# Performance work log

Hardware: AMD Instinct MI355X
Metric: run time of the kernel (lower is better)

The kernel has to match this reference:

```python
import jax, jax.numpy as jnp
import numpy as np
from jax import lax

EPS = 1e-8  # torch F.cosine_similarity default eps


def setup_inputs() -> dict:
    key = jax.random.key(0)
    k1, k2, k3 = jax.random.split(key, 3)
    B, S, D_in, D_out, W = 256, 10, 4096, 4096, 5
    x = jax.random.normal(k1, (B, S, D_in), dtype=jnp.float32)
    # Conv1d weight [out_channels, in_channels, kernel] with PyTorch-style init scale
    fan_in = D_in * W
    conv_w = jax.random.normal(k2, (D_out, D_in, W), dtype=jnp.float32) / np.sqrt(fan_in)
    conv_b = jax.random.normal(k3, (D_out,), dtype=jnp.float32) / np.sqrt(fan_in)
    return {"x": x, "conv_w": conv_w, "conv_b": conv_b}


def _cosine_weight(x):
    # x: [B, S, D]; central frame index = S//2 + 1 (as in the original code)
    S = x.shape[1]
    c = S // 2 + 1
    central = x[:, c, :]                               # [B, D]
    dots = jnp.einsum("bsd,bd->bs", x, central)        # [B, S]
    norms = jnp.sqrt(jnp.sum(x * x, axis=-1))          # [B, S]
    cnorm = norms[:, c]                                # [B]
    denom = jnp.maximum(norms, EPS) * jnp.maximum(cnorm, EPS)[:, None]
    w = dots / denom                                   # [B, S] (raw weights; normalization in source is dead code)
    return x * w[..., None]                            # [B, S, D]


def reference(x, conv_w, conv_b):
    xw = _cosine_weight(x)                             # [B, S, D_in]
    xc = jnp.transpose(xw, (0, 2, 1))                  # [B, D_in, S]
    y = lax.conv_general_dilated(
        xc, conv_w, window_strides=(1,), padding="VALID",
        dimension_numbers=("NCH", "OIH", "NCH"),
    )                                                  # [B, D_out, S-W+1]
    y = y + conv_b[None, :, None]
    return jnp.mean(y, axis=-1)                        # [B, D_out]
```

## Files before the change

### kernel.cpp

```cpp
#include <hip/hip_runtime.h>
#include <hip/hip_bf16.h>

typedef __hip_bfloat16 bf16;
typedef __attribute__((ext_vector_type(8))) __bf16 bf16x8;
typedef __attribute__((ext_vector_type(4))) __bf16 bf16x4;
typedef __attribute__((ext_vector_type(4))) float f32x4;

typedef const __attribute__((address_space(1))) void cgvoid;
typedef __attribute__((address_space(3))) void lvoid;

constexpr int B_ = 256, S_ = 10, D_ = 4096, W_ = 5;
constexpr int K_ = D_ * W_;
constexpr int M_ = 256, N_ = 4096;
constexpr int KS_ = 8;
constexpr int KPER = K_ / KS_;
constexpr int BK_ = 32;
constexpr int ITERS = KPER / BK_;
constexpr int TN_ = 64;
constexpr float EPSV = 1e-8f;

__global__ void detect_kernel(const unsigned short* __restrict__ xr, int* __restrict__ flag){
    int lane = threadIdx.x;
    int sane = 0;
    for (int i = lane; i < 2048; i += 64){
        unsigned short u = xr[i];
        int e = (u >> 7) & 0xFF;
        if ((e >= 97 && e <= 137) || ((u & 0x7FFF) == 0)) sane++;
    }
    #pragma unroll
    for (int off = 32; off > 0; off >>= 1) sane += __shfl_down(sane, off);
    if (lane == 0) *flag = (sane >= 1536) ? 1 : 0;
}

__global__ __launch_bounds__(512) void zw_kernel(const void* __restrict__ xv,
                                                 bf16* __restrict__ Z,
                                                 const int* __restrict__ flag){
    const bool isb = (*flag != 0);
    int b = blockIdx.x, t = threadIdx.x;
    int i0 = t * 8;
    float f[S_][8];
    if (isb){
        const __bf16* xb = (const __bf16*)xv + (size_t)b * S_ * D_ + i0;
        #pragma unroll
        for (int s = 0; s < S_; ++s){
            bf16x8 v = *(const bf16x8*)(xb + s * D_);
            #pragma unroll
            for (int j = 0; j < 8; ++j) f[s][j] = (float)v[j];
        }
    } else {
        const float* xb = (const float*)xv + (size_t)b * S_ * D_ + i0;
        #pragma unroll
        for (int s = 0; s < S_; ++s){
            float4 a = *(const float4*)(xb + s * D_);
            float4 c = *(const float4*)(xb + s * D_ + 4);
            f[s][0]=a.x; f[s][1]=a.y; f[s][2]=a.z; f[s][3]=a.w;
            f[s][4]=c.x; f[s][5]=c.y; f[s][6]=c.z; f[s][7]=c.w;
        }
    }
    float dsum[S_], nsum[S_];
    #pragma unroll
    for (int s = 0; s < S_; ++s){
        float d = 0.f, n = 0.f;
        #pragma unroll
        for (int j = 0; j < 8; ++j){ d += f[s][j] * f[6][j]; n += f[s][j] * f[s][j]; }
        dsum[s] = d; nsum[s] = n;
    }
    int lane = t & 63, wv = t >> 6;
    #pragma unroll
    for (int s = 0; s < S_; ++s){
        #pragma unroll
        for (int off = 32; off > 0; off >>= 1){
            dsum[s] += __shfl_down(dsum[s], off);
            nsum[s] += __shfl_down(nsum[s], off);
        }
    }
    __shared__ float sd[8][S_], sn[8][S_], wsh[S_];
    if (lane == 0){
        #pragma unroll
        for (int s = 0; s < S_; ++s){ sd[wv][s] = dsum[s]; sn[wv][s] = nsum[s]; }
    }
    __syncthreads();
    if (t < S_){
        float Dv = 0.f, Nv = 0.f;
        #pragma unroll
        for (int w2 = 0; w2 < 8; ++w2){ Dv += sd[w2][t]; Nv += sn[w2][t]; }
        sd[0][t] = Dv; sn[0][t] = sqrtf(Nv);
    }
    __syncthreads();
    if (t < S_){
        wsh[t] = sd[0][t] / (fmaxf(sn[0][t], EPSV) * fmaxf(sn[0][6], EPSV));
    }
    __syncthreads();
    float w_[S_];
    #pragma unroll
    for (int s = 0; s < S_; ++s) w_[s] = wsh[s];
    alignas(16) __bf16 zout[40];
    #pragma unroll
    for (int k = 0; k < W_; ++k){
        #pragma unroll
        for (int j = 0; j < 8; ++j){
            float acc = 0.f;
            #pragma unroll
            for (int t2 = 0; t2 < 6; ++t2) acc += w_[k + t2] * f[k + t2][j];
            zout[j * 5 + k] = (__bf16)acc;
        }
    }
    __bf16* zp = (__bf16*)Z + (size_t)b * K_ + (size_t)i0 * W_;
    #pragma unroll
    for (int v = 0; v < 5; ++v) *(bf16x8*)(zp + v * 8) = *(const bf16x8*)(zout + v * 8);
}

__global__ __launch_bounds__(512, 4) void gemm_kernel(const void* __restrict__ Wv,
                                                      const bf16* __restrict__ A,
                                                      float* __restrict__ P,
                                                      const int* __restrict__ flag){
    __shared__ alignas(16) __bf16 As[2][256 * BK_];
    __shared__ alignas(16) __bf16 Bs[2][TN_ * BK_];
    const bool isb = (*flag != 0);
    int tid = threadIdx.x, bid = blockIdx.x;
    int ks = bid & 7, nt = bid >> 3;
    int lane = tid & 63, wv = tid >> 6;
    int wm = wv & 3, wn = wv >> 2;
    int r16 = lane & 15, quad = lane >> 4;

    const __bf16* Ab   = (const __bf16*)A + (size_t)ks * KPER;
    const __bf16* Bb_b = (const __bf16*)Wv + (size_t)(nt * TN_) * K_ + (size_t)ks * KPER;
    const float*  Bb_f = (const float*) Wv + (size_t)(nt * TN_) * K_ + (size_t)ks * KPER;

    f32x4 acc[4][2];
    #pragma unroll
    for (int fm = 0; fm < 4; ++fm)
        #pragma unroll
        for (int fn = 0; fn < 2; ++fn) acc[fm][fn] = (f32x4){0.f, 0.f, 0.f, 0.f};

    #pragma unroll
    for (int r = 0; r < 2; ++r){
        int c = r * 512 + tid;
        const __bf16* src = Ab + (size_t)(c >> 2) * K_ + (c & 3) * 8;
        __builtin_amdgcn_global_load_lds((cgvoid*)src, (lvoid*)(&As[0][0] + c * 8), 16, 0, 0);
    }
    if (isb){
        if (tid < 256){
            const __bf16* src = Bb_b + (size_t)(tid >> 2) * K_ + (tid & 3) * 8;
            __builtin_amdgcn_global_load_lds((cgvoid*)src, (lvoid*)(&Bs[0][0] + tid * 8), 16, 0, 0);
        }
    } else {
        const float* src = Bb_f + (size_t)(tid >> 3) * K_ + (tid & 7) * 4;
        float4 f0 = *(const float4*)src;
        bf16x4 u;
        u[0] = (__bf16)f0.x; u[1] = (__bf16)f0.y; u[2] = (__bf16)f0.z; u[3] = (__bf16)f0.w;
        *(bf16x4*)(&Bs[0][(tid >> 3) * BK_ + (tid & 7) * 4]) = u;
    }
    __syncthreads();

    #pragma unroll 2
    for (int kk = 0; kk < ITERS; ++kk){
        int cur = kk & 1, nxt = cur ^ 1;
        bool havenext = (kk + 1 < ITERS);
        float4 f0;
        if (havenext){
            int kn = (kk + 1) * BK_;
            #pragma unroll
            for (int r = 0; r < 2; ++r){
                int c = r * 512 + tid;
                const __bf16* src = Ab + (size_t)(c >> 2) * K_ + (c & 3) * 8 + kn;
                __builtin_amdgcn_global_load_lds((cgvoid*)src, (lvoid*)(&As[nxt][0] + c * 8), 16, 0, 0);
            }
            if (isb){
                if (tid < 256){
                    const __bf16* src = Bb_b + (size_t)(tid >> 2) * K_ + (tid & 3) * 8 + kn;
                    __builtin_amdgcn_global_load_lds((cgvoid*)src, (lvoid*)(&Bs[nxt][0] + tid * 8), 16, 0, 0);
                }
            } else {
                const float* src = Bb_f + (size_t)(tid >> 3) * K_ + (tid & 7) * 4 + kn;
                f0 = *(const float4*)src;
            }
        }
        bf16x8 af[4], bfr[2];
        #pragma unroll
        for (int fm = 0; fm < 4; ++fm)
            af[fm] = *(const bf16x8*)(&As[cur][(wm * 64 + fm * 16 + r16) * BK_ + quad * 8]);
        #pragma unroll
        for (int fn = 0; fn < 2; ++fn)
            bfr[fn] = *(const bf16x8*)(&Bs[cur][(wn * 32 + fn * 16 + r16) * BK_ + quad * 8]);
        #pragma unroll
        for (int fm = 0; fm < 4; ++fm)
            #pragma unroll
            for (int fn = 0; fn < 2; ++fn)
                acc[fm][fn] = __builtin_amdgcn_mfma_f32_16x16x32_bf16(af[fm], bfr[fn], acc[fm][fn], 0, 0, 0);
        if (havenext && !isb){
            bf16x4 u;
            u[0] = (__bf16)f0.x; u[1] = (__bf16)f0.y; u[2] = (__bf16)f0.z; u[3] = (__bf16)f0.w;
            *(bf16x4*)(&Bs[nxt][(tid >> 3) * BK_ + (tid & 7) * 4]) = u;
        }
        __syncthreads();
    }

    float* Pb = P + (size_t)ks * M_ * N_;
    #pragma unroll
    for (int fm = 0; fm < 4; ++fm){
        #pragma unroll
        for (int fn = 0; fn < 2; ++fn){
            int n = nt * TN_ + wn * 32 + fn * 16 + r16;
            #pragma unroll
            for (int r = 0; r < 4; ++r){
                int m = wm * 64 + fm * 16 + quad * 4 + r;
                Pb[(size_t)m * N_ + n] = acc[fm][fn][r];
            }
        }
    }
}

__global__ __launch_bounds__(256) void reduce_kernel(const float* __restrict__ P,
                                                     const void* __restrict__ bias,
                                                     void* __restrict__ out,
                                                     const int* __restrict__ flag){
    const bool isb = (*flag != 0);
    int gid = blockIdx.x * 256 + threadIdx.x;
    int o4 = gid * 4;
    int n = o4 & (N_ - 1);
    float4 s = make_float4(0.f, 0.f, 0.f, 0.f);
    #pragma unroll
    for (int k2 = 0; k2 < KS_; ++k2){
        float4 p = *(const float4*)(P + (size_t)k2 * M_ * N_ + o4);
        s.x += p.x; s.y += p.y; s.z += p.z; s.w += p.w;
    }
    const float inv6 = 1.f / 6.f;
    float b0, b1, b2, b3;
    if (isb){
        const bf16* bp = (const bf16*)bias + n;
        b0 = __bfloat162float(bp[0]); b1 = __bfloat162float(bp[1]);
        b2 = __bfloat162float(bp[2]); b3 = __bfloat162float(bp[3]);
    } else {
        const float* bp = (const float*)bias + n;
        b0 = bp[0]; b1 = bp[1]; b2 = bp[2]; b3 = bp[3];
    }
    float r0 = s.x * inv6 + b0;
    float r1 = s.y * inv6 + b1;
    float r2 = s.z * inv6 + b2;
    float r3 = s.w * inv6 + b3;
    if (isb){
        bf16 h0 = __float2bfloat16(r0), h1 = __float2bfloat16(r1);
        bf16 h2 = __float2bfloat16(r2), h3 = __float2bfloat16(r3);
        ushort4 o;
        o.x = *(unsigned short*)&h0; o.y = *(unsigned short*)&h1;
        o.z = *(unsigned short*)&h2; o.w = *(unsigned short*)&h3;
        *(ushort4*)((unsigned short*)out + o4) = o;
    } else {
        *(float4*)((float*)out + o4) = make_float4(r0, r1, r2, r3);
    }
}

extern "C" void kernel_launch(void* const* d_in, const int* in_sizes, int n_in,
                              void* d_out, int out_size, void* d_ws, size_t ws_size,
                              hipStream_t stream){
    const void* x      = d_in[0];
    const void* conv_w = d_in[1];
    const void* conv_b = d_in[2];

    char* ws   = (char*)d_ws;
    int*  flag = (int*)ws;
    bf16* Z    = (bf16*)(ws + 16384);
    float* P   = (float*)(ws + 10502144);

    detect_kernel<<<1, 64, 0, stream>>>((const unsigned short*)x, flag);
    zw_kernel<<<256, 512, 0, stream>>>(x, Z, flag);
    gemm_kernel<<<512, 512, 0, stream>>>(conv_w, Z, P, flag);
    reduce_kernel<<<1024, 256, 0, stream>>>(P, conv_b, d_out, flag);
}
```

Before: 527.6 us.

## Replace split-K partial buffer with atomic accumulation into bias-initialized output

The zw kernel now writes the bias into an fp32 output buffer and folds the 1/6 mean scale into Z. The GEMM adds its split-K partials to that buffer with relaxed atomics, so the 8-way partial buffer write and reread in the reduce kernel go away. The final kernel only converts and copies. In exchange, each output element takes 8 atomic adds, which are uncoalesced per lane, and the summation order becomes nondeterministic.

```diff
diff --git a/kernel.cpp b/kernel.cpp
--- a/kernel.cpp
+++ b/kernel.cpp
@@ -34,6 +34,8 @@
 
 __global__ __launch_bounds__(512) void zw_kernel(const void* __restrict__ xv,
                                                  bf16* __restrict__ Z,
+                                                 float* __restrict__ O32,
+                                                 const void* __restrict__ bias,
                                                  const int* __restrict__ flag){
     const bool isb = (*flag != 0);
     int b = blockIdx.x, t = threadIdx.x;
@@ -57,6 +59,22 @@
             f[s][4]=c.x; f[s][5]=c.y; f[s][6]=c.z; f[s][7]=c.w;
         }
     }
+    {
+        float* orow = O32 + (size_t)b * N_ + i0;
+        if (isb){
+            const bf16* bp = (const bf16*)bias + i0;
+            float4 v0, v1;
+            v0.x = __bfloat162float(bp[0]); v0.y = __bfloat162float(bp[1]);
+            v0.z = __bfloat162float(bp[2]); v0.w = __bfloat162float(bp[3]);
+            v1.x = __bfloat162float(bp[4]); v1.y = __bfloat162float(bp[5]);
+            v1.z = __bfloat162float(bp[6]); v1.w = __bfloat162float(bp[7]);
+            *(float4*)orow = v0; *(float4*)(orow + 4) = v1;
+        } else {
+            const float* bp = (const float*)bias + i0;
+            *(float4*)orow = *(const float4*)bp;
+            *(float4*)(orow + 4) = *(const float4*)(bp + 4);
+        }
+    }
     float dsum[S_], nsum[S_];
     #pragma unroll
     for (int s = 0; s < S_; ++s){
@@ -94,6 +112,7 @@
     float w_[S_];
     #pragma unroll
     for (int s = 0; s < S_; ++s) w_[s] = wsh[s];
+    const float inv6 = 1.f / 6.f;
     alignas(16) __bf16 zout[40];
     #pragma unroll
     for (int k = 0; k < W_; ++k){
@@ -102,7 +121,7 @@
             float acc = 0.f;
             #pragma unroll
             for (int t2 = 0; t2 < 6; ++t2) acc += w_[k + t2] * f[k + t2][j];
-            zout[j * 5 + k] = (__bf16)acc;
+            zout[j * 5 + k] = (__bf16)(acc * inv6);
         }
     }
     __bf16* zp = (__bf16*)Z + (size_t)b * K_ + (size_t)i0 * W_;
@@ -112,7 +131,7 @@
 
 __global__ __launch_bounds__(512, 4) void gemm_kernel(const void* __restrict__ Wv,
                                                       const bf16* __restrict__ A,
-                                                      float* __restrict__ P,
+                                                      float* __restrict__ O32,
                                                       const int* __restrict__ flag){
     __shared__ alignas(16) __bf16 As[2][256 * BK_];
     __shared__ alignas(16) __bf16 Bs[2][TN_ * BK_];
@@ -196,7 +215,6 @@
         __syncthreads();
     }
 
-    float* Pb = P + (size_t)ks * M_ * N_;
     #pragma unroll
     for (int fm = 0; fm < 4; ++fm){
         #pragma unroll
@@ -205,49 +223,29 @@
             #pragma unroll
             for (int r = 0; r < 4; ++r){
                 int m = wm * 64 + fm * 16 + quad * 4 + r;
-                Pb[(size_t)m * N_ + n] = acc[fm][fn][r];
+                __hip_atomic_fetch_add(&O32[(size_t)m * N_ + n], acc[fm][fn][r],
+                                       __ATOMIC_RELAXED, __HIP_MEMORY_SCOPE_AGENT);
             }
         }
     }
 }
 
-__global__ __launch_bounds__(256) void reduce_kernel(const float* __restrict__ P,
-                                                     const void* __restrict__ bias,
-                                                     void* __restrict__ out,
-                                                     const int* __restrict__ flag){
+__global__ __launch_bounds__(256) void finalize_kernel(const float* __restrict__ O32,
+                                                       void* __restrict__ out,
+                                                       const int* __restrict__ flag){
     const bool isb = (*flag != 0);
     int gid = blockIdx.x * 256 + threadIdx.x;
     int o4 = gid * 4;
-    int n = o4 & (N_ - 1);
-    float4 s = make_float4(0.f, 0.f, 0.f, 0.f);
-    #pragma unroll
-    for (int k2 = 0; k2 < KS_; ++k2){
-        float4 p = *(const float4*)(P + (size_t)k2 * M_ * N_ + o4);
-        s.x += p.x; s.y += p.y; s.z += p.z; s.w += p.w;
-    }
-    const float inv6 = 1.f / 6.f;
-    float b0, b1, b2, b3;
+    float4 v = *(const float4*)(O32 + o4);
     if (isb){
-        const bf16* bp = (const bf16*)bias + n;
-        b0 = __bfloat162float(bp[0]); b1 = __bfloat162float(bp[1]);
-        b2 = __bfloat162float(bp[2]); b3 = __bfloat162float(bp[3]);
-    } else {
-        const float* bp = (const float*)bias + n;
-        b0 = bp[0]; b1 = bp[1]; b2 = bp[2]; b3 = bp[3];
-    }
-    float r0 = s.x * inv6 + b0;
-    float r1 = s.y * inv6 + b1;
-    float r2 = s.z * inv6 + b2;
-    float r3 = s.w * inv6 + b3;
-    if (isb){
-        bf16 h0 = __float2bfloat16(r0), h1 = __float2bfloat16(r1);
-        bf16 h2 = __float2bfloat16(r2), h3 = __float2bfloat16(r3);
+        bf16 h0 = __float2bfloat16(v.x), h1 = __float2bfloat16(v.y);
+        bf16 h2 = __float2bfloat16(v.z), h3 = __float2bfloat16(v.w);
         ushort4 o;
         o.x = *(unsigned short*)&h0; o.y = *(unsigned short*)&h1;
         o.z = *(unsigned short*)&h2; o.w = *(unsigned short*)&h3;
         *(ushort4*)((unsigned short*)out + o4) = o;
     } else {
-        *(float4*)((float*)out + o4) = make_float4(r0, r1, r2, r3);
+        *(float4*)((float*)out + o4) = v;
     }
 }
 
@@ -261,10 +259,10 @@
     char* ws   = (char*)d_ws;
     int*  flag = (int*)ws;
     bf16* Z    = (bf16*)(ws + 16384);
-    float* P   = (float*)(ws + 10502144);
+    float* O32 = (float*)(ws + 10502144);
 
     detect_kernel<<<1, 64, 0, stream>>>((const unsigned short*)x, flag);
-    zw_kernel<<<256, 512, 0, stream>>>(x, Z, flag);
-    gemm_kernel<<<512, 512, 0, stream>>>(conv_w, Z, P, flag);
-    reduce_kernel<<<1024, 256, 0, stream>>>(P, conv_b, d_out, flag);
-}
+    zw_kernel<<<256, 512, 0, stream>>>(x, Z, O32, conv_b, flag);
+    gemm_kernel<<<512, 512, 0, stream>>>(conv_w, Z, O32, flag);
+    finalize_kernel<<<1024, 256, 0, stream>>>(O32, d_out, flag);
+}
```

Result: no change. 535.0 us (+1.4%).
